# Kernel tuning notes

Hardware: AMD Instinct MI355X
Metric: run time of the kernel (lower is better)

Reference implementation:

```python
import jax, jax.numpy as jnp
import numpy as np

B, S, D, H, HD = 2, 2048, 2048, 16, 128

def _freqs_cis(dim, end, theta=10000.0):
    freqs = 1.0 / theta ** (np.arange(0, dim, 2, dtype=np.float32)[: dim // 2] / dim)
    t = np.arange(end, dtype=np.float32)
    f = np.outer(t, freqs).astype(np.float32)
    f = np.concatenate((f, f), axis=-1)
    return jnp.asarray(np.cos(f)), jnp.asarray(np.sin(f))

def _rotate_half(x):
    x1, x2 = x[..., : x.shape[-1] // 2], x[..., x.shape[-1] // 2 :]
    return jnp.concatenate((-x2, x1), axis=-1)

def setup_inputs() -> dict:
    key = jax.random.key(0)
    ks = jax.random.split(key, 5)
    x = jax.random.normal(ks[0], (B, S, D), jnp.float32)
    scale = 1.0 / np.sqrt(D)
    Wq = jax.random.normal(ks[1], (D, H, HD), jnp.float32) * scale
    Wk = jax.random.normal(ks[2], (D, H, HD), jnp.float32) * scale
    Wv = jax.random.normal(ks[3], (D, H, HD), jnp.float32) * scale
    Wo = jax.random.normal(ks[4], (H, HD, D), jnp.float32) * (1.0 / np.sqrt(D))
    mask = jnp.tril(jnp.ones((S, S), jnp.bool_))[None, None]  # causal [1,1,S,S]
    return {"x": x, "mask": mask, "Wq": Wq, "Wk": Wk, "Wv": Wv, "Wo": Wo}

def reference(x, mask, Wq, Wk, Wv, Wo):
    # QKV projections: [B,S,D] -> [B,S,H,HD]
    q = jnp.einsum('bsd,dhk->bshk', x, Wq)
    k = jnp.einsum('bsd,dhk->bshk', x, Wk)
    v = jnp.einsum('bsd,dhk->bshk', x, Wv)
    # RoPE
    cos, sin = _freqs_cis(HD, x.shape[1])
    cos = cos[None, :, None, :]
    sin = sin[None, :, None, :]
    q = q * cos + _rotate_half(q) * sin
    k = k * cos + _rotate_half(k) * sin
    # scaled dot-product attention
    scores = jnp.einsum('bqhk,bshk->bhqs', q, k) / jnp.sqrt(jnp.asarray(HD, q.dtype))
    big_neg = jnp.finfo(scores.dtype).min
    scores = jnp.where(mask, scores, big_neg)
    attn = jax.nn.softmax(scores, axis=-1)
    ctx = jnp.einsum('bhqs,bshk->bqhk', attn, v)
    # output projection contracting (heads, head_dim)
    return jnp.einsum('bqhk,hkd->bqd', ctx, Wo)
```

## Files before the change

kernel.cpp:

```cpp
#include <hip/hip_runtime.h>

typedef unsigned short u16;
typedef unsigned int u32;

constexpr int Bc = 2, Sc = 2048, Dc = 2048, Hc = 16, HDc = 128;

using short8 = __attribute__((ext_vector_type(8))) short;
using f32x4v = __attribute__((ext_vector_type(4))) float;

static __device__ __forceinline__ float bf2f(u16 v) { return __uint_as_float(((u32)v) << 16); }
static __device__ __forceinline__ u16 f2bf(float f) {
    u32 u = __float_as_uint(f);
    return (u16)((u + 0x7fffu + ((u >> 16) & 1u)) >> 16);
}

__device__ __forceinline__ void gll16(const u16* g, u16* l) {
    __builtin_amdgcn_global_load_lds((const __attribute__((address_space(1))) void*)g,
                                     (__attribute__((address_space(3))) void*)l, 16, 0, 0);
}

#define FENCE asm volatile("" ::: "memory")
#define BARX do { FENCE; __builtin_amdgcn_s_barrier(); FENCE; } while (0)

__global__ __launch_bounds__(256) void rope_tab_k(float* __restrict__ ctab, float* __restrict__ stab) {
    int idx = blockIdx.x * 256 + threadIdx.x;
    int s = idx >> 6, i = idx & 63;
    float freq = exp2f(-(float)i * 0.20762050593045952f);
    float ang = (float)s * freq;
    float c, sn;
    sincosf(ang, &sn, &c);
    ctab[idx] = c;
    stab[idx] = sn;
}

__global__ __launch_bounds__(256) void cvt_k(const float* __restrict__ in, u16* __restrict__ out, int n) {
    int i = (blockIdx.x * 256 + threadIdx.x) * 8;
    if (i >= n) return;
    float4 a = *(const float4*)(in + i);
    float4 b = *(const float4*)(in + i + 4);
    u16 r[8] = {f2bf(a.x), f2bf(a.y), f2bf(a.z), f2bf(a.w),
                f2bf(b.x), f2bf(b.y), f2bf(b.z), f2bf(b.w)};
    *(uint4*)(out + i) = *(uint4*)r;
}

__global__ __launch_bounds__(256) void tcvt3_k(const float* __restrict__ in0, const float* __restrict__ in1,
                                               const float* __restrict__ in2, u16* __restrict__ out,
                                               int R, int C) {
    __shared__ u16 tile[64][68];
    const float* in = (blockIdx.z == 0) ? in0 : (blockIdx.z == 1) ? in1 : in2;
    u16* o = out + (size_t)blockIdx.z * R * C;
    int bx = blockIdx.x * 64, by = blockIdx.y * 64;
    int t = threadIdx.x;
    int r = t >> 4, c4 = (t & 15) * 4;
    #pragma unroll
    for (int i = 0; i < 4; ++i) {
        int row = by + r + i * 16;
        float4 v = *(const float4*)(in + (size_t)row * C + bx + c4);
        u16* d = &tile[r + i * 16][c4];
        d[0] = f2bf(v.x); d[1] = f2bf(v.y); d[2] = f2bf(v.z); d[3] = f2bf(v.w);
    }
    __syncthreads();
    int oc = t >> 4, r4 = (t & 15) * 4;
    #pragma unroll
    for (int i = 0; i < 4; ++i) {
        int orow = oc + i * 16;
        u16 v[4] = {tile[r4][orow], tile[r4 + 1][orow], tile[r4 + 2][orow], tile[r4 + 3][orow]};
        *(uint2*)&o[(size_t)(bx + orow) * R + by + r4] = *(const uint2*)v;
    }
}


#define QT2(RB, KST, SB, LAST) do { \
    if (!(LAST)) { stage((KST), (SB)); \
        asm volatile("s_waitcnt vmcnt(4)" ::: "memory"); } \
    else asm volatile("s_waitcnt vmcnt(0)" ::: "memory"); \
    BARX; \
    short8 aF[4], bF[6]; \
    _Pragma("unroll") for (int m_ = 0; m_ < 4; ++m_) \
        aF[m_] = *(const short8*)((RB) + (wm * 64 + m_ * 16 + ln) * 32 + co); \
    _Pragma("unroll") for (int n_ = 0; n_ < 6; ++n_) \
        bF[n_] = *(const short8*)((RB) + 4096 + (wn * 96 + n_ * 16 + ln) * 32 + co); \
    asm volatile("s_waitcnt lgkmcnt(0)" ::: "memory"); \
    __builtin_amdgcn_s_setprio(1); \
    _Pragma("unroll") for (int m_ = 0; m_ < 4; ++m_) \
    _Pragma("unroll") for (int n_ = 0; n_ < 6; ++n_) \
        acc[m_][n_] = __builtin_amdgcn_mfma_f32_16x16x32_bf16(aF[m_], bF[n_], acc[m_][n_], 0, 0, 0); \
    __builtin_amdgcn_s_setprio(0); \
    BARX; \
} while (0)

__global__ __launch_bounds__(512, 2) void gemm_qkv2b(
        const u16* __restrict__ A, const u16* __restrict__ Bt,
        u16* __restrict__ Oq, u16* __restrict__ Ok, u16* __restrict__ Ov,
        const float* __restrict__ ctab, const float* __restrict__ stab) {
    __shared__ u16 SM[32768];
    constexpr int K = Dc;
    int t = threadIdx.x, wid = t >> 6, lane = t & 63;
    int wm = wid >> 2, wn = wid & 3;
    int ln = lane & 15, lq = lane >> 4;

    int lin = blockIdx.x;
    int swzb = (lin & 7) * 64 + (lin >> 3);
    int n0 = (swzb >> 5) * 384;
    int m0 = (swzb & 31) * 128;

    auto stage = [&](int kt, int b) {
        u16* Ad = SM + b * 16384;
        u16* Bd = SM + b * 16384 + 4096;
        {
            int row = t >> 2, cs = t & 3;
            gll16(A + (size_t)(m0 + row) * K + kt * 32 + ((cs ^ ((row >> 1) & 3)) << 3),
                  Ad + (wid * 64) * 8);
        }
        #pragma unroll
        for (int L = 0; L < 3; ++L) {
            int ci = L * 512 + t;
            int row = ci >> 2, cs = ci & 3;
            gll16(Bt + (size_t)(n0 + row) * K + kt * 32 + ((cs ^ ((row >> 1) & 3)) << 3),
                  Bd + (L * 512 + wid * 64) * 8);
        }
    };

    int co = ((lq ^ ((ln >> 1) & 3)) << 3);
    f32x4v acc[4][6] = {};

    stage(0, 0);

    #pragma unroll 1
    for (int kt = 0; kt < 62; kt += 2) {
        QT2(SM,         kt + 1, 1, 0);
        QT2(SM + 16384, kt + 2, 0, 0);
    }
    QT2(SM,         63, 1, 0);
    QT2(SM + 16384,  0, 0, 1);

    int b_ = m0 >> 11;
    int s0 = m0 & (Sc - 1);
    u16* Es = SM;
    const int ESTR = 130;

    for (int c = 0; c < 3; ++c) {
        #pragma unroll
        for (int nf = 0; nf < 6; ++nf) {
            int cg = wn * 96 + nf * 16;
            if ((cg >> 7) == c) {
                int col = cg & 127;
                #pragma unroll
                for (int mf = 0; mf < 4; ++mf)
                    #pragma unroll
                    for (int r = 0; r < 4; ++r)
                        Es[(wm * 64 + mf * 16 + (lq << 2) + r) * ESTR + col + ln] =
                            f2bf(acc[mf][nf][r]);
            }
        }
        __syncthreads();

        int gcol = n0 + c * 128;
        int which = gcol >> 11;
        int h = (gcol & 2047) >> 7;
        if (which < 2) {
            u16* dst0 = which ? Ok : Oq;
            int rh = t >> 2, h2 = t & 1, jh = (t >> 1) & 1;
            int s = s0 + rh;
            const u16* rowp = Es + rh * ESTR;
            const float* ct = ctab + (size_t)s * 64;
            const float* st = stab + (size_t)s * 64;
            u16* dp = dst0 + (((size_t)(b_ * Hc + h)) * Sc + s) * HDc + h2 * 64;
            #pragma unroll
            for (int j8 = jh * 32; j8 < jh * 32 + 32; j8 += 8) {
                uint4 aa = *(const uint4*)(rowp + j8);
                uint4 bb = *(const uint4*)(rowp + 64 + j8);
                const u16* ap8 = (const u16*)&aa;
                const u16* bp8 = (const u16*)&bb;
                float4 c0f = *(const float4*)(ct + j8);
                float4 c1f = *(const float4*)(ct + j8 + 4);
                float4 sn0 = *(const float4*)(st + j8);
                float4 sn1 = *(const float4*)(st + j8 + 4);
                float cc[8] = {c0f.x, c0f.y, c0f.z, c0f.w, c1f.x, c1f.y, c1f.z, c1f.w};
                float ss[8] = {sn0.x, sn0.y, sn0.z, sn0.w, sn1.x, sn1.y, sn1.z, sn1.w};
                u16 ov[8];
                #pragma unroll
                for (int e = 0; e < 8; ++e) {
                    float x1 = bf2f(ap8[e]), x2 = bf2f(bp8[e]);
                    ov[e] = h2 ? f2bf(x2 * cc[e] + x1 * ss[e]) : f2bf(x1 * cc[e] - x2 * ss[e]);
                }
                *(uint4*)(dp + j8) = *(const uint4*)ov;
            }
        } else {
            int d = t >> 2, sh = t & 3;
            u16* dp = Ov + (((size_t)(b_ * Hc + h)) * HDc + d) * Sc + s0 + sh * 32;
            #pragma unroll
            for (int r8 = 0; r8 < 32; r8 += 8) {
                u16 ov[8];
                #pragma unroll
                for (int e = 0; e < 8; ++e)
                    ov[e] = Es[(sh * 32 + r8 + e) * ESTR + d];
                *(uint4*)(dp + r8) = *(const uint4*)ov;
            }
        }
        __syncthreads();
    }
}


#define RDA8(P) do { _Pragma("unroll") for (int m_ = 0; m_ < 4; ++m_) { \
    aG[m_][0] = *(const short8*)((P) + m_ * 1024 + co0); \
    aG[m_][1] = *(const short8*)((P) + m_ * 1024 + co1); } } while (0)

#define RDB2(P, nh) do { _Pragma("unroll") for (int j_ = 0; j_ < 2; ++j_) { \
    bG[j_][0] = *(const short8*)((P) + ((nh) * 2 + j_) * 1024 + co0); \
    bG[j_][1] = *(const short8*)((P) + ((nh) * 2 + j_) * 1024 + co1); } } while (0)

#define MFQ8(nh) do { _Pragma("unroll") for (int m_ = 0; m_ < 4; ++m_) \
    _Pragma("unroll") for (int j_ = 0; j_ < 2; ++j_) { \
    f32x4v& c_ = acc[m_][(nh) * 2 + j_]; \
    c_ = __builtin_amdgcn_mfma_f32_16x16x32_bf16(aG[m_][0], bG[j_][0], c_, 0, 0, 0); \
    c_ = __builtin_amdgcn_mfma_f32_16x16x32_bf16(aG[m_][1], bG[j_][1], c_, 0, 0, 0); } } while (0)

#define PT(nh) do { BARX; \
    asm volatile("s_waitcnt lgkmcnt(0)" ::: "memory"); \
    __builtin_amdgcn_s_setprio(1); MFQ8(nh); __builtin_amdgcn_s_setprio(0); \
    BARX; } while (0)

#define KTILE(aRb, bRb, KST, ADST, BDST, VW) do { \
    RDA8(aRb); RDB2(bRb, 0); \
    if ((KST) >= 0) stageA(KST, ADST); \
    PT(0); \
    RDB2(bRb, 1); \
    if ((KST) >= 0) stageB(KST, BDST); \
    if ((VW) == 6) asm volatile("s_waitcnt vmcnt(6)" ::: "memory"); \
    else if ((VW) == 0) asm volatile("s_waitcnt vmcnt(0)" ::: "memory"); \
    PT(1); } while (0)

__global__ __launch_bounds__(512, 2) void gemm128_op(
        const u16* __restrict__ A, const u16* __restrict__ Bt, float* __restrict__ C2) {
    __shared__ u16 SM[73728];
    constexpr int K = Dc;
    constexpr int NT = 32;
    constexpr int N = Dc;
    int t = threadIdx.x, wid = t >> 6, lane = t & 63;
    int wm = wid >> 2, wn = wid & 3;
    int ln = lane & 15, lq = lane >> 4;

    int nx = gridDim.x;
    int lin = blockIdx.y * nx + blockIdx.x;
    int cpx = (nx * gridDim.y) >> 3;
    int swzb = (lin & 7) * cpx + (lin >> 3);
    int n0 = (swzb % nx) << 8;
    int m0 = (swzb / nx) << 7;

    u16* As0 = SM;
    u16* As1 = SM + 8192;
    u16* As2 = SM + 16384;
    u16* Bs0 = SM + 24576;
    u16* Bs1 = SM + 40960;
    u16* Bs2 = SM + 57344;

    auto stageA = [&](int kt, u16* dst) {
        #pragma unroll
        for (int L = 0; L < 2; ++L) {
            int ch16 = L * 512 + wid * 64 + lane;
            int row = ch16 >> 3, ch = ch16 & 7;
            gll16(A + (size_t)(m0 + row) * K + kt * 64 + ((ch ^ (row & 7)) << 3),
                  dst + (L * 512 + wid * 64) * 8);
        }
    };
    auto stageB = [&](int kt, u16* dst) {
        #pragma unroll
        for (int L = 0; L < 4; ++L) {
            int ch16 = L * 512 + wid * 64 + lane;
            int row = ch16 >> 3, ch = ch16 & 7;
            gll16(Bt + (size_t)(n0 + row) * K + kt * 64 + ((ch ^ (row & 7)) << 3),
                  dst + (L * 512 + wid * 64) * 8);
        }
    };

    const u16* aR0 = As0 + (wm * 64 + ln) * 64;
    const u16* aR1 = As1 + (wm * 64 + ln) * 64;
    const u16* aR2 = As2 + (wm * 64 + ln) * 64;
    const u16* bR0 = Bs0 + (wn * 64 + ln) * 64;
    const u16* bR1 = Bs1 + (wn * 64 + ln) * 64;
    const u16* bR2 = Bs2 + (wn * 64 + ln) * 64;
    int sw = ln & 7;
    int co0 = (lq ^ sw) << 3;
    int co1 = ((4 | lq) ^ sw) << 3;

    short8 aG[4][2], bG[2][2];
    f32x4v acc[4][4] = {};

    stageA(0, As0); stageB(0, Bs0);
    stageA(1, As1); stageB(1, Bs1);
    asm volatile("s_waitcnt vmcnt(6)" ::: "memory");
    BARX;

    for (int k3 = 0; k3 < NT - 2; k3 += 3) {
        KTILE(aR0, bR0, k3 + 2, As2, Bs2, 6);
        KTILE(aR1, bR1, k3 + 3, As0, Bs0, 6);
        KTILE(aR2, bR2, k3 + 4, As1, Bs1, 6);
    }
    KTILE(aR0, bR0, -1, As0, Bs0, 0);
    KTILE(aR1, bR1, -1, As0, Bs0, -1);

    int rb = m0 + wm * 64 + (lq << 2);
    int cb = n0 + wn * 64 + ln;
    #pragma unroll
    for (int mf = 0; mf < 4; ++mf)
        #pragma unroll
        for (int nf = 0; nf < 4; ++nf)
            #pragma unroll
            for (int r = 0; r < 4; ++r)
                C2[(size_t)(rb + mf * 16 + r) * N + cb + nf * 16] = acc[mf][nf][r];
}

__global__ __launch_bounds__(256) void fattn_k(const u16* __restrict__ Q, const u16* __restrict__ K,
                                               const u16* __restrict__ Vt, u16* __restrict__ ctx) {
    __shared__ u16 KsA[2 * 8192];
    __shared__ u16 VsA[2 * 8192];
    __shared__ u16 PsA[4 * 32 * 64];
    int t = threadIdx.x, wid = t >> 6, lane = t & 63;
    int bh = blockIdx.x;
    int yt = blockIdx.y;
    int qi = (yt < 8) ? yt : 23 - yt;
    int q0 = qi << 7;
    int wrow0 = q0 + wid * 32;
    const u16* Qb = Q + ((size_t)bh * Sc + wrow0) * HDc;
    const u16* Kb = K + (size_t)bh * Sc * HDc;
    const u16* Vb = Vt + (size_t)bh * HDc * Sc;
    int ln = lane & 15, lq = lane >> 4;
    u16* psw = PsA + wid * 2048;

    short8 aq[2][4];
    #pragma unroll
    for (int mf = 0; mf < 2; ++mf)
        #pragma unroll
        for (int ks = 0; ks < 4; ++ks)
            aq[mf][ks] = *(const short8*)(Qb + (size_t)(mf * 16 + ln) * HDc + ks * 32 + lq * 8);

    short8 onesb;
    {
        short v = (ln == 0) ? (short)0x3F80 : (short)0;
        #pragma unroll
        for (int e = 0; e < 8; ++e) onesb[e] = v;
    }

    f32x4v o[2][8] = {};
    f32x4v lacc[2] = {};

    const float sc = 0.08838834764831845f;
    const float SHIFT = 12.0f;
    int jendw = wrow0 + 31;
    int jendb = q0 + 127;
    int swz = (ln >> 1) & 3;

    auto stageKV = [&](int j0s, int buf) {
        u16* Kd = KsA + buf * 8192;
        u16* Vd = VsA + buf * 8192;
        #pragma unroll
        for (int i = 0; i < 4; ++i) {
            int p = (wid * 4 + i) * 64 + lane;
            int plane = p >> 8, key = (p >> 2) & 63;
            int qc = (p & 3) ^ ((key >> 1) & 3);
            gll16(Kb + (size_t)(j0s + key) * HDc + plane * 32 + qc * 8,
                  Kd + (size_t)(wid * 4 + i) * 512);
        }
        #pragma unroll
        for (int i = 0; i < 4; ++i) {
            int p = (wid * 4 + i) * 64 + lane;
            int plane = p >> 9, d = (p >> 2) & 127;
            int qc = (p & 3) ^ ((d >> 1) & 3);
            gll16(Vb + (size_t)d * Sc + j0s + plane * 32 + qc * 8,
                  Vd + (size_t)(wid * 4 + i) * 512);
        }
    };

    stageKV(0, 0);
    for (int j0 = 0; j0 <= jendb; j0 += 64) {
        int cur = (j0 >> 6) & 1;
        if (j0 + 64 <= jendb) {
            stageKV(j0 + 64, cur ^ 1);
            asm volatile("s_waitcnt vmcnt(8)" ::: "memory");
        } else {
            asm volatile("s_waitcnt vmcnt(0)" ::: "memory");
        }
        BARX;

        if (j0 <= jendw) {
            const u16* Kc = KsA + cur * 8192;
            const u16* Vc = VsA + cur * 8192;
            f32x4v sf[2][4] = {};
            #pragma unroll
            for (int ks = 0; ks < 4; ++ks)
                #pragma unroll
                for (int nf = 0; nf < 4; ++nf) {
                    short8 bk = *(const short8*)(Kc + ks * 2048 + (nf * 16 + ln) * 32 + ((lq ^ swz) << 3));
                    sf[0][nf] = __builtin_amdgcn_mfma_f32_16x16x32_bf16(aq[0][ks], bk, sf[0][nf], 0, 0, 0);
                    sf[1][nf] = __builtin_amdgcn_mfma_f32_16x16x32_bf16(aq[1][ks], bk, sf[1][nf], 0, 0, 0);
                }

            bool diag = (j0 + 63 > wrow0);
            #pragma unroll
            for (int mf = 0; mf < 2; ++mf) {
                int rowb = mf * 16 + (lq << 2);
                #pragma unroll
                for (int nf = 0; nf < 4; ++nf) {
                    int col = nf * 16 + ln;
                    int ck = col >> 3, cl = col & 7;
                    #pragma unroll
                    for (int r = 0; r < 4; ++r) {
                        float p = __expf(fmaf(sf[mf][nf][r], sc, -SHIFT));
                        if (diag && (j0 + col > wrow0 + rowb + r)) p = 0.f;
                        int row = rowb + r;
                        psw[row * 64 + ((ck ^ (row & 7)) << 3) + cl] = f2bf(p);
                    }
                }
            }

            short8 ap0[2][2];
            #pragma unroll
            for (int mf = 0; mf < 2; ++mf)
                #pragma unroll
                for (int ks = 0; ks < 2; ++ks)
                    ap0[mf][ks] = *(const short8*)(psw + (mf * 16 + ln) * 64 + (((ks * 4 + lq) ^ (ln & 7)) << 3));
            #pragma unroll
            for (int ks = 0; ks < 2; ++ks) {
                lacc[0] = __builtin_amdgcn_mfma_f32_16x16x32_bf16(ap0[0][ks], onesb, lacc[0], 0, 0, 0);
                lacc[1] = __builtin_amdgcn_mfma_f32_16x16x32_bf16(ap0[1][ks], onesb, lacc[1], 0, 0, 0);
                #pragma unroll
                for (int nd = 0; nd < 8; ++nd) {
                    short8 bv = *(const short8*)(Vc + ks * 4096 + (nd * 16 + ln) * 32 + ((lq ^ swz) << 3));
                    o[0][nd] = __builtin_amdgcn_mfma_f32_16x16x32_bf16(ap0[0][ks], bv, o[0][nd], 0, 0, 0);
                    o[1][nd] = __builtin_amdgcn_mfma_f32_16x16x32_bf16(ap0[1][ks], bv, o[1][nd], 0, 0, 0);
                }
            }
        }
        BARX;
    }

    int b = bh >> 4, h = bh & 15;
    #pragma unroll
    for (int mf = 0; mf < 2; ++mf)
        #pragma unroll
        for (int r = 0; r < 4; ++r) {
            float lv = __shfl(lacc[mf][r], lane & 48, 64);
            float inv = 1.0f / lv;
            int q = wrow0 + mf * 16 + (lq << 2) + r;
            u16* cp = ctx + (((size_t)(b * Sc + q)) * Hc + h) * HDc + ln;
            #pragma unroll
            for (int nd = 0; nd < 8; ++nd)
                cp[nd * 16] = f2bf(o[mf][nd][r] * inv);
        }
}

extern "C" void kernel_launch(void* const* d_in, const int* in_sizes, int n_in,
                              void* d_out, int out_size, void* d_ws, size_t ws_size,
                              hipStream_t stream) {
    (void)in_sizes; (void)n_in; (void)out_size; (void)ws_size;
    const float* x  = (const float*)d_in[0];
    const float* Wq = (const float*)d_in[2];
    const float* Wk = (const float*)d_in[3];
    const float* Wv = (const float*)d_in[4];
    const float* Wo = (const float*)d_in[5];

    char* w = (char*)d_ws;
    u16* Wt  = (u16*)w; w += (size_t)3 * Dc * Dc * 2;
    u16* Qb  = (u16*)w; w += (size_t)Bc * Hc * Sc * HDc * 2;
    u16* Kb  = (u16*)w; w += (size_t)Bc * Hc * Sc * HDc * 2;
    u16* Vb  = (u16*)w; w += (size_t)Bc * Hc * Sc * HDc * 2;
    u16* ctx = (u16*)w; w += (size_t)Bc * Sc * Hc * HDc * 2;
    float* ctab = (float*)w; w += (size_t)Sc * 64 * 4;
    float* stab = (float*)w; w += (size_t)Sc * 64 * 4;
    u16* xb = (u16*)d_out;

    rope_tab_k<<<dim3(Sc * 64 / 256), 256, 0, stream>>>(ctab, stab);

    int nx = Bc * Sc * Dc;
    cvt_k<<<dim3(nx / 2048), 256, 0, stream>>>(x, xb, nx);

    tcvt3_k<<<dim3(Dc / 64, Dc / 64, 3), 256, 0, stream>>>(Wq, Wk, Wv, Wt, Dc, Dc);
    gemm_qkv2b<<<dim3(512), 512, 0, stream>>>(xb, Wt, Qb, Kb, Vb, ctab, stab);

    fattn_k<<<dim3(Bc * Hc, Sc / 128), 256, 0, stream>>>(Qb, Kb, Vb, ctx);

    tcvt3_k<<<dim3(Dc / 64, Dc / 64, 1), 256, 0, stream>>>(Wo, Wo, Wo, Wt, Dc, Dc);
    gemm128_op<<<dim3(Dc / 256, (Bc * Sc) / 128), 512, 0, stream>>>(
        ctx, Wt, (float*)d_out);
}
```

Before: 396.4 us.

## Merge prep kernels and fold Wo transpose into attention launch; use exp2 softmax

Combines the RoPE-table, x-conversion and QKV weight transpose kernels into a single launch. It also appends the Wo transpose-convert blocks to the flash-attention grid, so they run alongside attention blocks instead of as a separate launch. Inside attention, the exponent is rewritten as exp2 with the log2(e) scale folded into the constants, and s_setprio is raised around the MFMA sections. This cuts launch count and idle tail time, at the cost of heterogeneous blocks sharing a grid and sharing LDS sizing.

Measured after the change: 403.1 us. Within noise of the previous version (+1.7%).

```diff
diff --git a/kernel.cpp b/kernel.cpp
--- a/kernel.cpp
+++ b/kernel.cpp
@@ -22,40 +22,13 @@
 #define FENCE asm volatile("" ::: "memory")
 #define BARX do { FENCE; __builtin_amdgcn_s_barrier(); FENCE; } while (0)
 
-__global__ __launch_bounds__(256) void rope_tab_k(float* __restrict__ ctab, float* __restrict__ stab) {
-    int idx = blockIdx.x * 256 + threadIdx.x;
-    int s = idx >> 6, i = idx & 63;
-    float freq = exp2f(-(float)i * 0.20762050593045952f);
-    float ang = (float)s * freq;
-    float c, sn;
-    sincosf(ang, &sn, &c);
-    ctab[idx] = c;
-    stab[idx] = sn;
-}
-
-__global__ __launch_bounds__(256) void cvt_k(const float* __restrict__ in, u16* __restrict__ out, int n) {
-    int i = (blockIdx.x * 256 + threadIdx.x) * 8;
-    if (i >= n) return;
-    float4 a = *(const float4*)(in + i);
-    float4 b = *(const float4*)(in + i + 4);
-    u16 r[8] = {f2bf(a.x), f2bf(a.y), f2bf(a.z), f2bf(a.w),
-                f2bf(b.x), f2bf(b.y), f2bf(b.z), f2bf(b.w)};
-    *(uint4*)(out + i) = *(uint4*)r;
-}
-
-__global__ __launch_bounds__(256) void tcvt3_k(const float* __restrict__ in0, const float* __restrict__ in1,
-                                               const float* __restrict__ in2, u16* __restrict__ out,
-                                               int R, int C) {
-    __shared__ u16 tile[64][68];
-    const float* in = (blockIdx.z == 0) ? in0 : (blockIdx.z == 1) ? in1 : in2;
-    u16* o = out + (size_t)blockIdx.z * R * C;
-    int bx = blockIdx.x * 64, by = blockIdx.y * 64;
-    int t = threadIdx.x;
+__device__ __forceinline__ void tcvt_body(const float* __restrict__ in, u16* __restrict__ o,
+                                          int bx, int by, u16 (*tile)[68], int t) {
     int r = t >> 4, c4 = (t & 15) * 4;
     #pragma unroll
     for (int i = 0; i < 4; ++i) {
         int row = by + r + i * 16;
-        float4 v = *(const float4*)(in + (size_t)row * C + bx + c4);
+        float4 v = *(const float4*)(in + (size_t)row * Dc + bx + c4);
         u16* d = &tile[r + i * 16][c4];
         d[0] = f2bf(v.x); d[1] = f2bf(v.y); d[2] = f2bf(v.z); d[3] = f2bf(v.w);
     }
@@ -65,7 +38,41 @@
     for (int i = 0; i < 4; ++i) {
         int orow = oc + i * 16;
         u16 v[4] = {tile[r4][orow], tile[r4 + 1][orow], tile[r4 + 2][orow], tile[r4 + 3][orow]};
-        *(uint2*)&o[(size_t)(bx + orow) * R + by + r4] = *(const uint2*)v;
+        *(uint2*)&o[(size_t)(bx + orow) * Dc + by + r4] = *(const uint2*)v;
+    }
+}
+
+__global__ __launch_bounds__(256) void prep_k(const float* __restrict__ x,
+                                              const float* __restrict__ Wq,
+                                              const float* __restrict__ Wk,
+                                              const float* __restrict__ Wv,
+                                              u16* __restrict__ xb, u16* __restrict__ Wt,
+                                              float* __restrict__ ctab, float* __restrict__ stab) {
+    __shared__ u16 tile[64][68];
+    int bid = blockIdx.x, t = threadIdx.x;
+    if (bid < 512) {
+        int idx = bid * 256 + t;
+        int s = idx >> 6, i = idx & 63;
+        float freq = exp2f(-(float)i * 0.20762050593045952f);
+        float ang = (float)s * freq;
+        float c, sn;
+        sincosf(ang, &sn, &c);
+        ctab[idx] = c;
+        stab[idx] = sn;
+    } else if (bid < 4608) {
+        int i = ((bid - 512) * 256 + t) * 8;
+        float4 a = *(const float4*)(x + i);
+        float4 b = *(const float4*)(x + i + 4);
+        u16 r[8] = {f2bf(a.x), f2bf(a.y), f2bf(a.z), f2bf(a.w),
+                    f2bf(b.x), f2bf(b.y), f2bf(b.z), f2bf(b.w)};
+        *(uint4*)(xb + i) = *(uint4*)r;
+    } else {
+        int id = bid - 4608;
+        int z = id >> 10;
+        int rem = id & 1023;
+        int bx = (rem & 31) * 64, by = (rem >> 5) * 64;
+        const float* in = (z == 0) ? Wq : (z == 1) ? Wk : Wv;
+        tcvt_body(in, Wt + (size_t)z * Dc * Dc, bx, by, tile, t);
     }
 }
 
@@ -202,7 +209,6 @@
     }
 }
 
-
 #define RDA8(P) do { _Pragma("unroll") for (int m_ = 0; m_ < 4; ++m_) { \
     aG[m_][0] = *(const short8*)((P) + m_ * 1024 + co0); \
     aG[m_][1] = *(const short8*)((P) + m_ * 1024 + co1); } } while (0)
@@ -312,14 +318,24 @@
                 C2[(size_t)(rb + mf * 16 + r) * N + cb + nf * 16] = acc[mf][nf][r];
 }
 
-__global__ __launch_bounds__(256) void fattn_k(const u16* __restrict__ Q, const u16* __restrict__ K,
-                                               const u16* __restrict__ Vt, u16* __restrict__ ctx) {
+__global__ __launch_bounds__(256) void fattn_tc(const u16* __restrict__ Q, const u16* __restrict__ K,
+                                                const u16* __restrict__ Vt, u16* __restrict__ ctx,
+                                                const float* __restrict__ Wo, u16* __restrict__ Wt) {
     __shared__ u16 KsA[2 * 8192];
     __shared__ u16 VsA[2 * 8192];
     __shared__ u16 PsA[4 * 32 * 64];
-    int t = threadIdx.x, wid = t >> 6, lane = t & 63;
-    int bh = blockIdx.x;
-    int yt = blockIdx.y;
+    int bid = blockIdx.x, t = threadIdx.x;
+
+    if (bid >= 512) {
+        int id = bid - 512;
+        int bx = (id & 31) * 64, by = (id >> 5) * 64;
+        tcvt_body(Wo, Wt, bx, by, (u16(*)[68])KsA, t);
+        return;
+    }
+
+    int wid = t >> 6, lane = t & 63;
+    int bh = bid & 31;
+    int yt = bid >> 5;
     int qi = (yt < 8) ? yt : 23 - yt;
     int q0 = qi << 7;
     int wrow0 = q0 + wid * 32;
@@ -346,8 +362,8 @@
     f32x4v o[2][8] = {};
     f32x4v lacc[2] = {};
 
-    const float sc = 0.08838834764831845f;
-    const float SHIFT = 12.0f;
+    const float sc2 = 0.12751726861f;
+    const float SHIFT2 = 17.312340490667f;
     int jendw = wrow0 + 31;
     int jendb = q0 + 127;
     int swz = (ln >> 1) & 3;
@@ -388,6 +404,7 @@
             const u16* Kc = KsA + cur * 8192;
             const u16* Vc = VsA + cur * 8192;
             f32x4v sf[2][4] = {};
+            __builtin_amdgcn_s_setprio(1);
             #pragma unroll
             for (int ks = 0; ks < 4; ++ks)
                 #pragma unroll
@@ -396,6 +413,7 @@
                     sf[0][nf] = __builtin_amdgcn_mfma_f32_16x16x32_bf16(aq[0][ks], bk, sf[0][nf], 0, 0, 0);
                     sf[1][nf] = __builtin_amdgcn_mfma_f32_16x16x32_bf16(aq[1][ks], bk, sf[1][nf], 0, 0, 0);
                 }
+            __builtin_amdgcn_s_setprio(0);
 
             bool diag = (j0 + 63 > wrow0);
             #pragma unroll
@@ -407,7 +425,7 @@
                     int ck = col >> 3, cl = col & 7;
                     #pragma unroll
                     for (int r = 0; r < 4; ++r) {
-                        float p = __expf(fmaf(sf[mf][nf][r], sc, -SHIFT));
+                        float p = exp2f(fmaf(sf[mf][nf][r], sc2, -SHIFT2));
                         if (diag && (j0 + col > wrow0 + rowb + r)) p = 0.f;
                         int row = rowb + r;
                         psw[row * 64 + ((ck ^ (row & 7)) << 3) + cl] = f2bf(p);
@@ -421,6 +439,7 @@
                 #pragma unroll
                 for (int ks = 0; ks < 2; ++ks)
                     ap0[mf][ks] = *(const short8*)(psw + (mf * 16 + ln) * 64 + (((ks * 4 + lq) ^ (ln & 7)) << 3));
+            __builtin_amdgcn_s_setprio(1);
             #pragma unroll
             for (int ks = 0; ks < 2; ++ks) {
                 lacc[0] = __builtin_amdgcn_mfma_f32_16x16x32_bf16(ap0[0][ks], onesb, lacc[0], 0, 0, 0);
@@ -432,6 +451,7 @@
                     o[1][nd] = __builtin_amdgcn_mfma_f32_16x16x32_bf16(ap0[1][ks], bv, o[1][nd], 0, 0, 0);
                 }
             }
+            __builtin_amdgcn_s_setprio(0);
         }
         BARX;
     }
@@ -471,17 +491,12 @@
     float* stab = (float*)w; w += (size_t)Sc * 64 * 4;
     u16* xb = (u16*)d_out;
 
-    rope_tab_k<<<dim3(Sc * 64 / 256), 256, 0, stream>>>(ctab, stab);
-
-    int nx = Bc * Sc * Dc;
-    cvt_k<<<dim3(nx / 2048), 256, 0, stream>>>(x, xb, nx);
-
-    tcvt3_k<<<dim3(Dc / 64, Dc / 64, 3), 256, 0, stream>>>(Wq, Wk, Wv, Wt, Dc, Dc);
+    prep_k<<<dim3(7680), 256, 0, stream>>>(x, Wq, Wk, Wv, xb, Wt, ctab, stab);
+
     gemm_qkv2b<<<dim3(512), 512, 0, stream>>>(xb, Wt, Qb, Kb, Vb, ctab, stab);
 
-    fattn_k<<<dim3(Bc * Hc, Sc / 128), 256, 0, stream>>>(Qb, Kb, Vb, ctx);
-
-    tcvt3_k<<<dim3(Dc / 64, Dc / 64, 1), 256, 0, stream>>>(Wo, Wo, Wo, Wt, Dc, Dc);
+    fattn_tc<<<dim3(1536), 256, 0, stream>>>(Qb, Kb, Vb, ctx, Wo, Wt);
+
     gemm128_op<<<dim3(Dc / 256, (Bc * Sc) / 128), 512, 0, stream>>>(
         ctx, Wt, (float*)d_out);
 }
```
